# Kernel optimization log

Hardware: AMD Instinct MI355X
Metric: run time of the kernel (lower is better)

Reference implementation:

```python
import jax, jax.numpy as jnp
import numpy as np
import math

# static config (mirrors Model.__init__)
NUM_SEGMENTS = 4
TILE = 32
NUM_SEQS = 8
Q_LEN = 128           # query tokens per sequence (uniform)
SEQ_LEN = 2048        # total seq len (context + query)
NUM_Q_HEADS = 32
NUM_KV_HEADS = 8
HEAD_SIZE = 128       # == head_size_padded (required for the torch code to type-check)
BLK_SIZE = 16
MAX_BLOCKS = SEQ_LEN // BLK_SIZE
NUM_BLKS = NUM_SEQS * MAX_BLOCKS


def setup_inputs() -> dict:
    key = jax.random.key(0)
    k1, k2, k3, k4 = jax.random.split(key, 4)
    num_tokens = NUM_SEQS * Q_LEN
    query = jax.random.normal(k1, (num_tokens, NUM_Q_HEADS, HEAD_SIZE), jnp.float32)
    # torch indexes key_cache[pb, kv, :, off, 0] -> 5D with trailing singleton
    key_cache = jax.random.normal(k2, (NUM_BLKS, NUM_KV_HEADS, HEAD_SIZE, BLK_SIZE, 1), jnp.float32)
    value_cache = jax.random.normal(k3, (NUM_BLKS, NUM_KV_HEADS, HEAD_SIZE, BLK_SIZE), jnp.float32)
    # scattered (permuted) physical block assignment, vLLM-style
    block_tables = jax.random.permutation(k4, NUM_BLKS).reshape(NUM_SEQS, MAX_BLOCKS).astype(jnp.int32)
    seq_lens = jnp.full((NUM_SEQS,), SEQ_LEN, dtype=jnp.int32)
    query_start_len = jnp.arange(NUM_SEQS + 1, dtype=jnp.int32) * Q_LEN
    return {
        "query": query,
        "key_cache": key_cache,
        "value_cache": value_cache,
        "block_tables": block_tables,
        "seq_lens": seq_lens,
        "query_start_len": query_start_len,
        "scale": 1.0 / math.sqrt(HEAD_SIZE),
        "k_scale": 1.0,
        "v_scale": 1.0,
        "softcap": 30.0,
    }


def _paged_segmented_attention(query, key_cache, value_cache, block_tables, seq_lens, scale, softcap):
    S, M = block_tables.shape
    T, H, D = query.shape
    Hkv = key_cache.shape[1]
    G = H // Hkv                  # queries per kv head (GQA)
    B = key_cache.shape[3]
    Q = T // S                    # uniform query length per sequence
    L = M * B                     # KV length covered by the block table
    # block-table gather of paged KV -> [S, Hkv, L, D]
    k_all = key_cache[block_tables][..., 0]                              # [S, M, Hkv, D, B]
    k_all = jnp.transpose(k_all, (0, 2, 1, 4, 3)).reshape(S, Hkv, L, D)
    v_all = jnp.transpose(value_cache[block_tables], (0, 2, 1, 4, 3)).reshape(S, Hkv, L, D)
    q = query.reshape(S, Q, Hkv, G, D).astype(jnp.float32)
    scores = scale * jnp.einsum('sqhgd,shld->shgql', q, k_all.astype(jnp.float32))  # [S,Hkv,G,Q,L]
    if softcap > 0:
        scores = softcap * jnp.tanh(scores / softcap)
    ctx = seq_lens - Q                                                   # context length per seq [S]
    qabs = ctx[:, None] + jnp.arange(Q)[None, :]                         # absolute q positions [S,Q]
    kpos = jnp.arange(L)
    causal = kpos[None, None, :] <= qabs[:, :, None]                     # [S,Q,L]
    # keys per segment = tiles_per_segment * 32, per sequence
    span = (-(-seq_lens // (NUM_SEGMENTS * TILE))) * TILE                # [S]
    neg_inf = jnp.float32(-jnp.inf)
    v32 = v_all.astype(jnp.float32)
    outs = []
    for seg in range(NUM_SEGMENTS):                                      # small fixed loop
        seg_mask = (kpos[None, :] >= seg * span[:, None]) & (kpos[None, :] < (seg + 1) * span[:, None])  # [S,L]
        mask = (causal & seg_mask[:, None, :])[:, None, None, :, :]      # [S,1,1,Q,L]
        masked = jnp.where(mask, scores, neg_inf)
        m = masked.max(axis=-1)
        m_safe = jnp.where(m > neg_inf, m, 0.0)                          # torch's zero-clamp of -inf max
        p = jnp.exp(masked - m_safe[..., None])                          # [S,Hkv,G,Q,L]
        # NOTE: torch returns the UNNORMALIZED accumulator (expsum is discarded)
        acc = jnp.einsum('shgql,shld->shgqd', p, v32)
        outs.append(acc)
    out = jnp.stack(outs, axis=-2)                                       # [S,Hkv,G,Q,NSEG,D]
    out = jnp.transpose(out, (0, 3, 1, 2, 4, 5)).reshape(T, H, NUM_SEGMENTS, D)
    return out.astype(query.dtype)


def reference(query, key_cache, value_cache, block_tables, seq_lens, query_start_len, scale, k_scale, v_scale, softcap):
    # fp32 cache path: k_scale/v_scale dequantization is a no-op (torch applies it only for fp8 caches).
    # query_start_len is consistent with uniform Q_LEN per sequence (used implicitly via reshape).
    return _paged_segmented_attention(query, key_cache, value_cache, block_tables, seq_lens,
                                      float(scale), float(softcap))
```

## Files before the change

kernel.cpp:

```cpp
#include <hip/hip_runtime.h>

#define NSEQ   8
#define QLEN   128
#define NQH    32
#define NKVH   8
#define GQ     4
#define HD     128
#define BLK    16
#define MAXBLK 128
#define LTOT   2048
#define NSEGC  4
#define TILEC  32

typedef __attribute__((ext_vector_type(8)))  short  shortx8;
typedef __attribute__((ext_vector_type(16))) float  floatx16;
typedef __attribute__((ext_vector_type(4)))  float  fx4;
typedef __attribute__((ext_vector_type(4)))  int    intx4;
typedef __attribute__((ext_vector_type(2)))  __bf16 bf16x2;

__device__ __forceinline__ int pk2(float a, float b) {
    bf16x2 t; t[0] = (__bf16)a; t[1] = (__bf16)b;
    return __builtin_bit_cast(int, t);
}

__global__ __launch_bounds__(256) void psa_kernel(
    const float* __restrict__ query,
    const float* __restrict__ key_cache,
    const float* __restrict__ value_cache,
    const int*   __restrict__ block_tables,
    const int*   __restrict__ seq_lens,
    const float* __restrict__ scale_p,
    const float* __restrict__ softcap_p,
    float* __restrict__ out)
{
    __shared__ __align__(16) short kbuf[2][16][32][8];
    __shared__ __align__(16) short vbuf[2][4][128][8];

    const int bi  = blockIdx.x;
    const int g   = bi >> 8;
    const int rem = bi & 255;
    const int seg = rem & 3;
    const int h   = (rem >> 2) & 7;
    const int s   = rem >> 5;

    const int tid  = threadIdx.x;
    const int w    = tid >> 6;
    const int lane = tid & 63;
    const int lo   = lane & 31;
    const int hi   = lane >> 5;

    const float NEG_INF = -__builtin_inff();
    const float scale   = *scale_p;
    const float softcap = *softcap_p;
    const int   seq     = seq_lens[s];
    const int   ctx     = seq - QLEN;
    const int   span    = ((seq + NSEGC * TILEC - 1) / (NSEGC * TILEC)) * TILEC;
    const int   seg_start = seg * span;
    int seg_len = LTOT - seg_start;
    if (seg_len > span) seg_len = span;
    const int NT = (seg_len > 0) ? ((seg_len + 31) >> 5) : 0;

    const float LOG2E = 1.4426950408889634f;
    const bool  do_cap = (softcap > 0.0f);
    const float c1 = do_cap ? (2.0f * LOG2E / softcap) : 0.0f;
    const float c2 = do_cap ? (softcap * LOG2E) : 0.0f;

    const int qb    = w * 32;
    const int qrow  = qb + lo;
    const int q_off = ((s * QLEN + qrow) * NQH + h * GQ + g) * HD;
    shortx8 qfrag[8];
#pragma unroll
    for (int ks = 0; ks < 8; ++ks) {
        const float* qp = query + q_off + ks * 16 + hi * 8;
        fx4 a = *(const fx4*)qp;
        fx4 b = *(const fx4*)(qp + 4);
        intx4 w4 = { pk2(a[0] * scale, a[1] * scale), pk2(a[2] * scale, a[3] * scale),
                     pk2(b[0] * scale, b[1] * scale), pk2(b[2] * scale, b[3] * scale) };
        qfrag[ks] = __builtin_bit_cast(shortx8, w4);
    }

    const int bt_base = s * MAXBLK;

    float kreg[2][8];
    fx4   vreg[2][2];
    const int kb  = tid & 31;
    const int kdc = tid >> 5;
    const int vd  = tid & 127;
    const int vlh = tid >> 7;

    auto stage_load = [&](int nt) {
        {
            int l_glob = seg_start + nt * 32 + kb;
            if (l_glob >= LTOT) l_glob = LTOT - 1;
            const int pb = block_tables[bt_base + (l_glob >> 4)];
            const float* kp = key_cache + (pb * NKVH + h) * (HD * BLK) + (l_glob & 15);
#pragma unroll
            for (int ic = 0; ic < 2; ++ic)
#pragma unroll
                for (int j = 0; j < 8; ++j)
                    kreg[ic][j] = kp[((kdc + ic * 8) * 8 + j) * BLK];
        }
        {
#pragma unroll
            for (int ic = 0; ic < 2; ++ic) {
                const int lslab = vlh + ic * 2;
                int l_glob = seg_start + nt * 32 + lslab * 8;
                if (l_glob >= LTOT) l_glob = LTOT - 8;
                const int pb = block_tables[bt_base + (l_glob >> 4)];
                const float* vp = value_cache + ((pb * NKVH + h) * HD + vd) * BLK + (l_glob & 15);
                vreg[ic][0] = *(const fx4*)vp;
                vreg[ic][1] = *(const fx4*)(vp + 4);
            }
        }
    };
    auto stage_write = [&](int bb_) {
#pragma unroll
        for (int ic = 0; ic < 2; ++ic) {
            intx4 w4 = { pk2(kreg[ic][0], kreg[ic][1]), pk2(kreg[ic][2], kreg[ic][3]),
                         pk2(kreg[ic][4], kreg[ic][5]), pk2(kreg[ic][6], kreg[ic][7]) };
            *(intx4*)(&kbuf[bb_][kdc + ic * 8][kb][0]) = w4;
        }
#pragma unroll
        for (int ic = 0; ic < 2; ++ic) {
            intx4 w4 = { pk2(vreg[ic][0][0], vreg[ic][0][1]), pk2(vreg[ic][0][2], vreg[ic][0][3]),
                         pk2(vreg[ic][1][0], vreg[ic][1][1]), pk2(vreg[ic][1][2], vreg[ic][1][3]) };
            *(intx4*)(&vbuf[bb_][vlh + ic * 2][vd][0]) = w4;
        }
    };

    floatx16 acc[4];
#pragma unroll
    for (int dt = 0; dt < 4; ++dt)
#pragma unroll
        for (int i = 0; i < 16; ++i) acc[dt][i] = 0.0f;
    float m_run = NEG_INF;

    if (NT > 0) { stage_load(0); stage_write(0); }

    for (int nt = 0; nt < NT; ++nt) {
        const int bb = nt & 1;
        __syncthreads();
        const bool pre = (nt + 1 < NT);
        if (pre) stage_load(nt + 1);

        const int tile_l0 = seg_start + nt * 32;
        const bool need_mask = (tile_l0 + 31 > ctx + qb) || (nt * 32 + 31 >= seg_len);

        floatx16 c;
#pragma unroll
        for (int i = 0; i < 16; ++i) c[i] = 0.0f;
#pragma unroll
        for (int ks = 0; ks < 8; ++ks) {
            shortx8 af = *(const shortx8*)(&kbuf[bb][ks * 2 + hi][lo][0]);
            c = __builtin_amdgcn_mfma_f32_32x32x16_bf16(af, qfrag[ks], c, 0, 0, 0);
        }

        float z[16];
        float mloc = NEG_INF;
#pragma unroll
        for (int r = 0; r < 16; ++r) {
            const float si = c[r];
            float zz;
            if (do_cap) {
                const float u  = __builtin_amdgcn_exp2f(si * c1);
                const float rr = __builtin_amdgcn_rcpf(u + 1.0f);
                zz = c2 - (2.0f * c2) * rr;
            } else {
                zz = si * LOG2E;
            }
            if (need_mask) {
                const int key   = (r & 3) + 8 * (r >> 2) + 4 * hi;
                const int l_loc = nt * 32 + key;
                const bool ok = (l_loc < seg_len) && (tile_l0 + key <= ctx + qb + lo);
                zz = ok ? zz : NEG_INF;
            }
            z[r] = zz;
            mloc = fmaxf(mloc, zz);
        }
        mloc  = fmaxf(mloc, __shfl_xor(mloc, 32, 64));
        m_run = fmaxf(m_run, mloc);

        int A[8];
#pragma unroll
        for (int i = 0; i < 8; ++i)
            A[i] = pk2(__builtin_amdgcn_exp2f(z[2 * i]),
                       __builtin_amdgcn_exp2f(z[2 * i + 1]));
        auto s0 = __builtin_amdgcn_permlane32_swap(A[0], A[2], false, false);
        auto s1 = __builtin_amdgcn_permlane32_swap(A[1], A[3], false, false);
        auto s2 = __builtin_amdgcn_permlane32_swap(A[4], A[6], false, false);
        auto s3 = __builtin_amdgcn_permlane32_swap(A[5], A[7], false, false);
        intx4 w0 = { (int)s0[0], (int)s1[0], (int)s0[1], (int)s1[1] };
        intx4 w1 = { (int)s2[0], (int)s3[0], (int)s2[1], (int)s3[1] };
        shortx8 pf[2] = { __builtin_bit_cast(shortx8, w0),
                          __builtin_bit_cast(shortx8, w1) };

#pragma unroll
        for (int ks2 = 0; ks2 < 2; ++ks2) {
            const int slab = ks2 * 2 + hi;
#pragma unroll
            for (int dt = 0; dt < 4; ++dt) {
                shortx8 vf = *(const shortx8*)(&vbuf[bb][slab][dt * 32 + lo][0]);
                acc[dt] = __builtin_amdgcn_mfma_f32_32x32x16_bf16(pf[ks2], vf, acc[dt], 0, 0, 0);
            }
        }

        if (pre) stage_write(bb ^ 1);
    }

    const float scv = (m_run == NEG_INF) ? 0.0f : __builtin_amdgcn_exp2f(-m_run);
    const int out_base = ((s * QLEN + qb) * NQH + (h * GQ + g)) * (NSEGC * HD) + seg * HD + lo;
#pragma unroll
    for (int r = 0; r < 16; ++r) {
        const int row = (r & 3) + 8 * (r >> 2) + 4 * hi;
        const float sc = __shfl(scv, row, 64);
        const int ob = out_base + row * (NQH * NSEGC * HD);
#pragma unroll
        for (int dt = 0; dt < 4; ++dt)
            out[ob + dt * 32] = acc[dt][r] * sc;
    }
}

extern "C" void kernel_launch(void* const* d_in, const int* in_sizes, int n_in,
                              void* d_out, int out_size, void* d_ws, size_t ws_size,
                              hipStream_t stream) {
    const float* query        = (const float*)d_in[0];
    const float* key_cache    = (const float*)d_in[1];
    const float* value_cache  = (const float*)d_in[2];
    const int*   block_tables = (const int*)d_in[3];
    const int*   seq_lens     = (const int*)d_in[4];
    const float* scale_p      = (const float*)d_in[6];
    const float* softcap_p    = (const float*)d_in[9];

    psa_kernel<<<dim3(1024), dim3(256), 0, stream>>>(
        query, key_cache, value_cache, block_tables, seq_lens,
        scale_p, softcap_p, (float*)d_out);
}
```

Before: 244.2 us.

## Load V fragments directly from global into registers, skip LDS staging

Removes the V shared-memory buffer. Each wave now loads its V MFMA B-operand fragments straight from the paged value cache into registers, in two halves per tile, and converts them to bf16 in place. K staging is reworked into a deeper pipeline: the block-table lookup and the K data load run two tiles ahead and are written to LDS one tile ahead. Launch bounds now request 3 blocks per SM. This cuts LDS traffic and capacity, but each wave issues its own V global loads, so V is loaded redundantly across the 4 waves. The V loads also sit on the critical path right before the PV MFMAs, which risks exposed latency.

```diff
diff --git a/kernel.cpp b/kernel.cpp
--- a/kernel.cpp
+++ b/kernel.cpp
@@ -23,7 +23,7 @@
     return __builtin_bit_cast(int, t);
 }
 
-__global__ __launch_bounds__(256) void psa_kernel(
+__global__ __launch_bounds__(256, 3) void psa_kernel(
     const float* __restrict__ query,
     const float* __restrict__ key_cache,
     const float* __restrict__ value_cache,
@@ -34,7 +34,6 @@
     float* __restrict__ out)
 {
     __shared__ __align__(16) short kbuf[2][16][32][8];
-    __shared__ __align__(16) short vbuf[2][4][128][8];
 
     const int bi  = blockIdx.x;
     const int g   = bi >> 8;
@@ -82,49 +81,44 @@
     const int bt_base = s * MAXBLK;
 
     float kreg[2][8];
-    fx4   vreg[2][2];
+    int   pbK;
     const int kb  = tid & 31;
     const int kdc = tid >> 5;
-    const int vd  = tid & 127;
-    const int vlh = tid >> 7;
-
-    auto stage_load = [&](int nt) {
-        {
-            int l_glob = seg_start + nt * 32 + kb;
-            if (l_glob >= LTOT) l_glob = LTOT - 1;
-            const int pb = block_tables[bt_base + (l_glob >> 4)];
-            const float* kp = key_cache + (pb * NKVH + h) * (HD * BLK) + (l_glob & 15);
-#pragma unroll
-            for (int ic = 0; ic < 2; ++ic)
-#pragma unroll
-                for (int j = 0; j < 8; ++j)
-                    kreg[ic][j] = kp[((kdc + ic * 8) * 8 + j) * BLK];
-        }
-        {
-#pragma unroll
-            for (int ic = 0; ic < 2; ++ic) {
-                const int lslab = vlh + ic * 2;
-                int l_glob = seg_start + nt * 32 + lslab * 8;
-                if (l_glob >= LTOT) l_glob = LTOT - 8;
-                const int pb = block_tables[bt_base + (l_glob >> 4)];
-                const float* vp = value_cache + ((pb * NKVH + h) * HD + vd) * BLK + (l_glob & 15);
-                vreg[ic][0] = *(const fx4*)vp;
-                vreg[ic][1] = *(const fx4*)(vp + 4);
-            }
-        }
-    };
-    auto stage_write = [&](int bb_) {
+
+    auto btK_load = [&](int nt) {
+        int lK = seg_start + nt * 32 + kb;
+        if (lK >= LTOT) lK = LTOT - 1;
+        pbK = block_tables[bt_base + (lK >> 4)];
+    };
+    auto k_data_load = [&](int nt) {
+        int l_glob = seg_start + nt * 32 + kb;
+        if (l_glob >= LTOT) l_glob = LTOT - 1;
+        const float* kp = key_cache + (pbK * NKVH + h) * (HD * BLK) + (l_glob & 15);
+#pragma unroll
+        for (int ic = 0; ic < 2; ++ic)
+#pragma unroll
+            for (int j = 0; j < 8; ++j)
+                kreg[ic][j] = kp[((kdc + ic * 8) * 8 + j) * BLK];
+    };
+    auto k_stage_write = [&](int bb_) {
 #pragma unroll
         for (int ic = 0; ic < 2; ++ic) {
             intx4 w4 = { pk2(kreg[ic][0], kreg[ic][1]), pk2(kreg[ic][2], kreg[ic][3]),
                          pk2(kreg[ic][4], kreg[ic][5]), pk2(kreg[ic][6], kreg[ic][7]) };
             *(intx4*)(&kbuf[bb_][kdc + ic * 8][kb][0]) = w4;
         }
-#pragma unroll
-        for (int ic = 0; ic < 2; ++ic) {
-            intx4 w4 = { pk2(vreg[ic][0][0], vreg[ic][0][1]), pk2(vreg[ic][0][2], vreg[ic][0][3]),
-                         pk2(vreg[ic][1][0], vreg[ic][1][1]), pk2(vreg[ic][1][2], vreg[ic][1][3]) };
-            *(intx4*)(&vbuf[bb_][vlh + ic * 2][vd][0]) = w4;
+    };
+
+    auto v_issue = [&](int nt, int ks2, fx4 (&vf)[4][2]) {
+        int lb = seg_start + nt * 32 + (ks2 * 2 + hi) * 8;
+        if (lb >= LTOT) lb = LTOT - 8;
+        const int pb = block_tables[bt_base + (lb >> 4)];
+        const float* vbase = value_cache + (pb * NKVH + h) * (HD * BLK) + (lb & 15);
+#pragma unroll
+        for (int dt = 0; dt < 4; ++dt) {
+            const float* vp = vbase + (dt * 32 + lo) * BLK;
+            vf[dt][0] = *(const fx4*)vp;
+            vf[dt][1] = *(const fx4*)(vp + 4);
         }
     };
 
@@ -135,13 +129,18 @@
         for (int i = 0; i < 16; ++i) acc[dt][i] = 0.0f;
     float m_run = NEG_INF;
 
-    if (NT > 0) { stage_load(0); stage_write(0); }
+    if (NT > 0) {
+        btK_load(0); k_data_load(0); k_stage_write(0);
+        if (NT > 1) { btK_load(1); k_data_load(1); }
+    }
 
     for (int nt = 0; nt < NT; ++nt) {
         const int bb = nt & 1;
         __syncthreads();
-        const bool pre = (nt + 1 < NT);
-        if (pre) stage_load(nt + 1);
+        if (nt + 1 < NT) k_stage_write(bb ^ 1);
+
+        fx4 vf0[4][2];
+        v_issue(nt, 0, vf0);
 
         const int tile_l0 = seg_start + nt * 32;
         const bool need_mask = (tile_l0 + 31 > ctx + qb) || (nt * 32 + 31 >= seg_len);
@@ -154,6 +153,8 @@
             shortx8 af = *(const shortx8*)(&kbuf[bb][ks * 2 + hi][lo][0]);
             c = __builtin_amdgcn_mfma_f32_32x32x16_bf16(af, qfrag[ks], c, 0, 0, 0);
         }
+
+        if (nt + 2 < NT) btK_load(nt + 2);
 
         float z[16];
         float mloc = NEG_INF;
@@ -195,16 +196,25 @@
                           __builtin_bit_cast(shortx8, w1) };
 
 #pragma unroll
-        for (int ks2 = 0; ks2 < 2; ++ks2) {
-            const int slab = ks2 * 2 + hi;
-#pragma unroll
-            for (int dt = 0; dt < 4; ++dt) {
-                shortx8 vf = *(const shortx8*)(&vbuf[bb][slab][dt * 32 + lo][0]);
-                acc[dt] = __builtin_amdgcn_mfma_f32_32x32x16_bf16(pf[ks2], vf, acc[dt], 0, 0, 0);
-            }
-        }
-
-        if (pre) stage_write(bb ^ 1);
+        for (int dt = 0; dt < 4; ++dt) {
+            intx4 wv = { pk2(vf0[dt][0][0], vf0[dt][0][1]), pk2(vf0[dt][0][2], vf0[dt][0][3]),
+                         pk2(vf0[dt][1][0], vf0[dt][1][1]), pk2(vf0[dt][1][2], vf0[dt][1][3]) };
+            acc[dt] = __builtin_amdgcn_mfma_f32_32x32x16_bf16(
+                pf[0], __builtin_bit_cast(shortx8, wv), acc[dt], 0, 0, 0);
+        }
+
+        fx4 vf1[4][2];
+        v_issue(nt, 1, vf1);
+
+#pragma unroll
+        for (int dt = 0; dt < 4; ++dt) {
+            intx4 wv = { pk2(vf1[dt][0][0], vf1[dt][0][1]), pk2(vf1[dt][0][2], vf1[dt][0][3]),
+                         pk2(vf1[dt][1][0], vf1[dt][1][1]), pk2(vf1[dt][1][2], vf1[dt][1][3]) };
+            acc[dt] = __builtin_amdgcn_mfma_f32_32x32x16_bf16(
+                pf[1], __builtin_bit_cast(shortx8, wv), acc[dt], 0, 0, 0);
+        }
+
+        if (nt + 2 < NT) k_data_load(nt + 2);
     }
 
     const float scv = (m_run == NEG_INF) ? 0.0f : __builtin_amdgcn_exp2f(-m_run);
```

Result: slower. 499.9 us (+104.7%).
